# Performance work log

Measured on AMD Instinct MI355X. Metric: run time of the kernel, lower is better.

The kernel has to match this reference:

```python
import jax, jax.numpy as jnp
import numpy as np
import math

B, S, D, H = 4, 2048, 1024, 16
DK = D // H  # 64


def setup_inputs() -> dict:
    key = jax.random.key(0)
    ks = jax.random.split(key, 10)
    scale = 1.0 / math.sqrt(D)
    inp = {
        "context_sequence": jax.random.normal(ks[0], (B, S, D), dtype=jnp.float32),
        "value_sequence": jax.random.normal(ks[1], (B, S, D), dtype=jnp.float32),
        "mask": jax.random.randint(ks[2], (S, S), 0, 2, dtype=jnp.int32),
        # stacked per-head projection params: [H, D, DK] weights, [H, DK] biases
        "Wq": jax.random.uniform(ks[3], (H, D, DK), jnp.float32, -scale, scale),
        "bq": jnp.zeros((H, DK), jnp.float32),
        "Wk": jax.random.uniform(ks[4], (H, D, DK), jnp.float32, -scale, scale),
        "bk": jnp.zeros((H, DK), jnp.float32),
        "Wv": jax.random.uniform(ks[5], (H, D, DK), jnp.float32, -scale, scale),
        "bv": jnp.zeros((H, DK), jnp.float32),
        "Wo": jax.random.uniform(ks[6], (D, D), jnp.float32, -scale, scale),
        "bo": jnp.zeros((D,), jnp.float32),
    }
    return inp


def reference(context_sequence, value_sequence, mask, Wq, bq, Wk, bk, Wv, bv, Wo, bo):
    # per-head projections batched over heads: [B,H,S,DK]
    Q = jnp.einsum("bsd,hdk->bhsk", context_sequence, Wq) + bq[None, :, None, :]
    K = jnp.einsum("bsd,hdk->bhsk", context_sequence, Wk) + bk[None, :, None, :]
    V = jnp.einsum("bsd,hdk->bhsk", value_sequence, Wv) + bv[None, :, None, :]
    scores = jnp.einsum("bhsk,bhtk->bhst", Q, K) / math.sqrt(DK)
    scores = jnp.where(mask[None, None, :, :] == 1, jnp.float32(-1e9), scores)
    attn = jax.nn.softmax(scores, axis=-1)
    out = jnp.einsum("bhst,bhtk->bhsk", attn, V)  # [B,H,S,DK]
    concat = out.transpose(0, 2, 1, 3).reshape(B, S, D)  # heads concatenated
    # output projection (dropout is identity in eval mode)
    return concat @ Wo.T + bo
```

## Files before the change

kernel.cpp:

```cpp
#include <hip/hip_runtime.h>
#include <hip/hip_bf16.h>

#define DEVI __device__ __forceinline__

typedef __attribute__((ext_vector_type(8))) short bf16x8;
typedef __attribute__((ext_vector_type(4))) float f32x4;
typedef unsigned short u16;
typedef unsigned long long u64;


DEVI void async16(const void* g, const void* l) {
  __builtin_amdgcn_global_load_lds(
      (const __attribute__((address_space(1))) unsigned int*)g,
      (__attribute__((address_space(3))) unsigned int*)l, 16, 0, 0);
}

DEVI u16 f2bf(float x) {
  unsigned int u = __float_as_uint(x);
  return (u16)((u + 0x7fffu + ((u >> 16) & 1u)) >> 16);
}

DEVI float fast_exp2(float x) {
#if __has_builtin(__builtin_amdgcn_exp2f)
  return __builtin_amdgcn_exp2f(x);
#else
  return exp2f(x);
#endif
}

DEVI unsigned pk_bf16(unsigned hi, unsigned lo) {
#if __has_builtin(__builtin_amdgcn_perm)
  return __builtin_amdgcn_perm(hi, lo, 0x07060302u);
#else
  return (hi & 0xffff0000u) | (lo >> 16);
#endif
}

DEVI unsigned mk2(unsigned b, int k) {
  return ((((b >> k) & 1u) ? 0u : 0x0000FFFFu) | (((b >> (k + 1)) & 1u) ? 0u : 0xFFFF0000u));
}


__global__ __launch_bounds__(256) void prep_kernel(
    const float* __restrict__ ctx, const float* __restrict__ val, const int* __restrict__ msk,
    const float* __restrict__ Wq, const float* __restrict__ Wk, const float* __restrict__ Wv,
    const float* __restrict__ Wo, const float* __restrict__ bq, const float* __restrict__ bk,
    u16* __restrict__ Xc, u16* __restrict__ Xv, u16* __restrict__ Wqt, u16* __restrict__ Wkt,
    u16* __restrict__ Wvt, u16* __restrict__ WoB, u64* __restrict__ mbits, float* __restrict__ bqk) {
  __shared__ float tile[64 * 69];
  const int blk = blockIdx.x, tid = threadIdx.x;
  if (blk < 16384) {
    const float* src = (blk < 8192) ? ctx : val;
    u16* dst = (blk < 8192) ? Xc : Xv;
    int i = (blk & 8191) * 256 + tid;
    float4 v = ((const float4*)src)[i];
    ushort4 o;
    o.x = f2bf(v.x); o.y = f2bf(v.y); o.z = f2bf(v.z); o.w = f2bf(v.w);
    ((ushort4*)dst)[i] = o;
  } else if (blk < 17408) {
    int i = (blk - 16384) * 256 + tid;
    float4 v = ((const float4*)Wo)[i];
    ushort4 o;
    o.x = f2bf(v.x); o.y = f2bf(v.y); o.z = f2bf(v.z); o.w = f2bf(v.w);
    ((ushort4*)WoB)[i] = o;
  } else if (blk < 18176) {
    int t = blk - 17408;
    int mat = t >> 8, r = t & 255, h = r >> 4, d0 = (r & 15) * 64;
    const float* Ws = (mat == 0) ? Wq : (mat == 1) ? Wk : Wv;
    u16* Wd = (mat == 0) ? Wqt : (mat == 1) ? Wkt : Wvt;
    const int dg = tid & 15, rg = tid >> 4;
#pragma unroll
    for (int i = 0; i < 4; i++) {
      int dr = rg + i * 16;
      float4 v = *(const float4*)&Ws[((size_t)(h * 1024 + d0 + dr)) * 64 + dg * 4];
      tile[dr * 69 + dg * 4 + 0] = v.x;
      tile[dr * 69 + dg * 4 + 1] = v.y;
      tile[dr * 69 + dg * 4 + 2] = v.z;
      tile[dr * 69 + dg * 4 + 3] = v.w;
    }
    __syncthreads();
#pragma unroll
    for (int i = 0; i < 4; i++) {
      int k = rg + i * 16;
      ushort4 o;
      o.x = f2bf(tile[(dg * 4 + 0) * 69 + k]);
      o.y = f2bf(tile[(dg * 4 + 1) * 69 + k]);
      o.z = f2bf(tile[(dg * 4 + 2) * 69 + k]);
      o.w = f2bf(tile[(dg * 4 + 3) * 69 + k]);
      *(ushort4*)&Wd[(size_t)(h * 64 + k) * 1024 + d0 + dg * 4] = o;
    }
  } else if (blk < 34560) {
    int gid = (blk - 18176) * 256 + tid;
    u64 bal = __ballot(msk[gid] == 1);
    if ((tid & 63) == 0) mbits[(size_t)((gid >> 6) & 31) * 2048 + (gid >> 11)] = bal;
  } else {
    int i = (blk - 34560) * 256 + tid;
    bqk[i] = (i < 1024) ? bq[i] : bk[i - 1024];
  }
}


__global__ __launch_bounds__(256) void qkv_gemm(const u16* __restrict__ Xc, const u16* __restrict__ Xv,
                                                const u16* __restrict__ Wqkt, const u16* __restrict__ Wvt,
                                                const float* __restrict__ bqk, const float* __restrict__ bvv,
                                                u16* __restrict__ QKb, u16* __restrict__ Vtg, float qscale) {
  __shared__ __align__(16) u16 As[128 * 32];
  __shared__ __align__(16) u16 Bs[128 * 32];
  const int tid = threadIdx.x;
  const int w = tid >> 6, lane = tid & 63, quad = lane >> 4, lc = lane & 15;
  const int K = 1024;
  const bool isV = blockIdx.y >= 16;
  const int m0 = blockIdx.x * 128;
  const int n0 = (isV ? (blockIdx.y - 16) : blockIdx.y) * 128;
  const u16* A  = isV ? Xv : Xc;
  const u16* Bt = isV ? Wvt : Wqkt;
  const float* bias = isV ? bvv : bqk;
  const int wrow = (w >> 1) * 64, wcol = (w & 1) * 64;
  const int srow = tid >> 2, sc = tid & 3;
  const u16* Ag = A + (size_t)(m0 + srow) * K + sc * 8;
  const u16* Bg = Bt + (size_t)(n0 + srow) * K + sc * 8;
  u16* Asw = As + w * 512;
  u16* Bsw = Bs + w * 512;

  f32x4 acc[4][4] = {};
  for (int k0 = 0; k0 < K; k0 += 32) {
    async16(Ag + k0, Asw);
    async16(Ag + k0 + (size_t)64 * K, Asw + 2048);
    async16(Bg + k0, Bsw);
    async16(Bg + k0 + (size_t)64 * K, Bsw + 2048);
    __syncthreads();
    bf16x8 af[4], bfr[4];
#pragma unroll
    for (int rt = 0; rt < 4; rt++) af[rt] = *(const bf16x8*)&As[(wrow + rt * 16 + lc) * 32 + quad * 8];
#pragma unroll
    for (int ct = 0; ct < 4; ct++) bfr[ct] = *(const bf16x8*)&Bs[(wcol + ct * 16 + lc) * 32 + quad * 8];
#pragma unroll
    for (int rt = 0; rt < 4; rt++)
#pragma unroll
      for (int ct = 0; ct < 4; ct++)
        acc[rt][ct] = __builtin_amdgcn_mfma_f32_16x16x32_bf16(af[rt], bfr[ct], acc[rt][ct], 0, 0, 0);
    __syncthreads();
  }
#pragma unroll
  for (int ct = 0; ct < 4; ct++) {
    int col = n0 + wcol + ct * 16 + lc;
    float bv = bias[col];
    float os = (!isV && col < 1024) ? qscale : 1.0f;
#pragma unroll
    for (int rt = 0; rt < 4; rt++) {
      if (isV) {
        int trow = m0 + wrow + rt * 16 + quad * 4;
        ushort4 pk;
        pk.x = f2bf(acc[rt][ct][0] + bv);
        pk.y = f2bf(acc[rt][ct][1] + bv);
        pk.z = f2bf(acc[rt][ct][2] + bv);
        pk.w = f2bf(acc[rt][ct][3] + bv);
        size_t off = ((size_t)(trow >> 11) * 1024 + col) * 2048 + (trow & 2047);
        *(ushort4*)(Vtg + off) = pk;
      } else {
#pragma unroll
        for (int r = 0; r < 4; r++) {
          int row = m0 + wrow + rt * 16 + quad * 4 + r;
          QKb[(size_t)row * 2048 + col] = f2bf((acc[rt][ct][r] + bv) * os);
        }
      }
    }
  }
}


__global__ __launch_bounds__(256, 4) void attn_kernel(const u16* __restrict__ QK, const u16* __restrict__ Vt,
                                                      const u64* __restrict__ mbits, u16* __restrict__ AO) {
  __shared__ __align__(16) u16 Ks[2][4096];
  __shared__ __align__(16) u16 Vs[2][4096];
  __shared__ uint4 Tbl[256];
  const int S = 2048, D = 1024, QS = 2048;
  const int tid = threadIdx.x, w = tid >> 6, lane = tid & 63, quad = lane >> 4, lc = lane & 15;
  const int q0 = blockIdx.x * 128;
  const int b = blockIdx.y >> 4, h = blockIdx.y & 15;
  const size_t baseq = (size_t)b * S * QS + (size_t)h * 64;
  const size_t vbase = (size_t)blockIdx.y * 64 * S;
  const int sr = lane >> 3, gch = (lane & 7) ^ sr, lx = lc & 7;
  u16* Ksq = (u16*)Ks;

  {
    unsigned bv = (unsigned)tid;
    uint4 e;
    e.x = mk2(bv, 0); e.y = mk2(bv, 2); e.z = mk2(bv, 4); e.w = mk2(bv, 6);
    Tbl[bv] = e;
  }

#pragma unroll
  for (int i = 0; i < 4; i++) {
    const u16* g = QK + baseq + (size_t)(q0 + w * 32 + i * 8 + sr) * QS + gch * 8;
    async16(g, Ksq + w * 2048 + i * 512);
  }
  const int kperm = 32 * (w & 1) + 4 * (w >> 1) + 8 * (sr >> 2) + (sr & 3);
  const u16* Kg0 = QK + baseq + 1024 + (size_t)kperm * QS + gch * 8;
  const u16* Vg0 = Vt + vbase + (size_t)(w * 16 + sr) * S + gch * 8;
  __syncthreads();

  bf16x8 aq[2][2];
#pragma unroll
  for (int s = 0; s < 2; s++)
#pragma unroll
    for (int ks = 0; ks < 2; ks++)
      aq[s][ks] = *(const bf16x8*)&Ksq[w * 2048 + (s * 16 + lc) * 64 + (((ks * 4 + quad) ^ lx) << 3)];
  __syncthreads();

  async16(Kg0, Ks[0] + w * 1024);
  async16(Kg0 + (size_t)16 * QS, Ks[0] + w * 1024 + 512);
  async16(Vg0, Vs[0] + w * 1024);
  async16(Vg0 + (size_t)8 * S, Vs[0] + w * 1024 + 512);

  const u64* mptr = mbits + (size_t)(q0 + w * 32 + lc);
  const int sh8 = quad << 3;

  bf16x8 ones;
#pragma unroll
  for (int j = 0; j < 8; j++) ones[j] = (short)0x3F80;

  const f32x4 z = {};
  f32x4 acco[2][4] = {};
  f32x4 accl[2] = {};

  for (int t0 = 0; t0 < S; t0 += 64) {
    const int cur = (t0 >> 6) & 1;
    __syncthreads();
    if (t0 + 64 < S) {
      const u16* Kg = Kg0 + (size_t)(t0 + 64) * QS;
      const u16* Vg = Vg0 + (t0 + 64);
      async16(Kg, Ks[cur ^ 1] + w * 1024);
      async16(Kg + (size_t)16 * QS, Ks[cur ^ 1] + w * 1024 + 512);
      async16(Vg, Vs[cur ^ 1] + w * 1024);
      async16(Vg + (size_t)8 * S, Vs[cur ^ 1] + w * 1024 + 512);
    }

    u64 mw0 = mptr[(size_t)(t0 >> 6) * 2048];
    u64 mw1 = mptr[(size_t)(t0 >> 6) * 2048 + 16];

    f32x4 sacc[2][4];
    __builtin_amdgcn_s_setprio(1);
#pragma unroll
    for (int ct = 0; ct < 4; ct++) {
      bf16x8 bk = *(const bf16x8*)&Ks[cur][(ct * 16 + lc) * 64 + ((quad ^ lx) << 3)];
      sacc[0][ct] = __builtin_amdgcn_mfma_f32_16x16x32_bf16(bk, aq[0][0], z, 0, 0, 0);
      sacc[1][ct] = __builtin_amdgcn_mfma_f32_16x16x32_bf16(bk, aq[1][0], z, 0, 0, 0);
    }
#pragma unroll
    for (int ct = 0; ct < 4; ct++) {
      bf16x8 bk = *(const bf16x8*)&Ks[cur][(ct * 16 + lc) * 64 + (((4 + quad) ^ lx) << 3)];
      sacc[0][ct] = __builtin_amdgcn_mfma_f32_16x16x32_bf16(bk, aq[0][1], sacc[0][ct], 0, 0, 0);
      sacc[1][ct] = __builtin_amdgcn_mfma_f32_16x16x32_bf16(bk, aq[1][1], sacc[1][ct], 0, 0, 0);
    }
    __builtin_amdgcn_s_setprio(0);

#pragma unroll
    for (int s = 0; s < 2; s++) {
      const u64 mw = s ? mw1 : mw0;
      uint4 ma = Tbl[((unsigned)mw >> sh8) & 255u];
      uint4 mb = Tbl[((unsigned)(mw >> 32) >> sh8) & 255u];
      unsigned pu[4][4];
#pragma unroll
      for (int ct = 0; ct < 4; ct++)
#pragma unroll
        for (int r = 0; r < 4; r++)
          pu[ct][r] = __float_as_uint(fast_exp2(sacc[s][ct][r]));
      union { unsigned u[4]; bf16x8 v; } f0, f1;
      f0.u[0] = pk_bf16(pu[0][1], pu[0][0]) & ma.x;
      f0.u[1] = pk_bf16(pu[0][3], pu[0][2]) & ma.y;
      f0.u[2] = pk_bf16(pu[2][1], pu[2][0]) & ma.z;
      f0.u[3] = pk_bf16(pu[2][3], pu[2][2]) & ma.w;
      f1.u[0] = pk_bf16(pu[1][1], pu[1][0]) & mb.x;
      f1.u[1] = pk_bf16(pu[1][3], pu[1][2]) & mb.y;
      f1.u[2] = pk_bf16(pu[3][1], pu[3][0]) & mb.z;
      f1.u[3] = pk_bf16(pu[3][3], pu[3][2]) & mb.w;

      __builtin_amdgcn_s_setprio(1);
#pragma unroll
      for (int ct = 0; ct < 4; ct++) {
        bf16x8 bv = *(const bf16x8*)&Vs[cur][(ct * 16 + lc) * 64 + ((quad ^ lx) << 3)];
        acco[s][ct] = __builtin_amdgcn_mfma_f32_16x16x32_bf16(f0.v, bv, acco[s][ct], 0, 0, 0);
      }
      accl[s] = __builtin_amdgcn_mfma_f32_16x16x32_bf16(f0.v, ones, accl[s], 0, 0, 0);
#pragma unroll
      for (int ct = 0; ct < 4; ct++) {
        bf16x8 bv = *(const bf16x8*)&Vs[cur][(ct * 16 + lc) * 64 + (((4 + quad) ^ lx) << 3)];
        acco[s][ct] = __builtin_amdgcn_mfma_f32_16x16x32_bf16(f1.v, bv, acco[s][ct], 0, 0, 0);
      }
      accl[s] = __builtin_amdgcn_mfma_f32_16x16x32_bf16(f1.v, ones, accl[s], 0, 0, 0);
      __builtin_amdgcn_s_setprio(0);
    }
  }

#pragma unroll
  for (int s = 0; s < 2; s++)
#pragma unroll
    for (int r = 0; r < 4; r++) {
      float inv = 1.0f / accl[s][r];
      size_t row = (size_t)b * S + q0 + w * 32 + s * 16 + quad * 4 + r;
#pragma unroll
      for (int ct = 0; ct < 4; ct++)
        AO[row * D + h * 64 + ct * 16 + lc] = f2bf(acco[s][ct][r] * inv);
    }
}


__global__ __launch_bounds__(256) void out_gemm(const u16* __restrict__ A, const u16* __restrict__ Bt,
                                                const float* __restrict__ bias, float* __restrict__ C) {
  __shared__ __align__(16) u16 As[128 * 32];
  __shared__ __align__(16) u16 Bs[128 * 32];
  const int tid = threadIdx.x;
  const int w = tid >> 6, lane = tid & 63, quad = lane >> 4, lc = lane & 15;
  const int K = 1024, N = 1024;
  const int m0 = blockIdx.x * 128, n0 = blockIdx.y * 128;
  const int wrow = (w >> 1) * 64, wcol = (w & 1) * 64;
  const int srow = tid >> 2, sc = tid & 3;
  const u16* Ag = A + (size_t)(m0 + srow) * K + sc * 8;
  const u16* Bg = Bt + (size_t)(n0 + srow) * K + sc * 8;
  u16* Asw = As + w * 512;
  u16* Bsw = Bs + w * 512;

  f32x4 acc[4][4] = {};
  for (int k0 = 0; k0 < K; k0 += 32) {
    async16(Ag + k0, Asw);
    async16(Ag + k0 + (size_t)64 * K, Asw + 2048);
    async16(Bg + k0, Bsw);
    async16(Bg + k0 + (size_t)64 * K, Bsw + 2048);
    __syncthreads();
    bf16x8 af[4], bfr[4];
#pragma unroll
    for (int rt = 0; rt < 4; rt++) af[rt] = *(const bf16x8*)&As[(wrow + rt * 16 + lc) * 32 + quad * 8];
#pragma unroll
    for (int ct = 0; ct < 4; ct++) bfr[ct] = *(const bf16x8*)&Bs[(wcol + ct * 16 + lc) * 32 + quad * 8];
#pragma unroll
    for (int rt = 0; rt < 4; rt++)
#pragma unroll
      for (int ct = 0; ct < 4; ct++)
        acc[rt][ct] = __builtin_amdgcn_mfma_f32_16x16x32_bf16(af[rt], bfr[ct], acc[rt][ct], 0, 0, 0);
    __syncthreads();
  }
#pragma unroll
  for (int ct = 0; ct < 4; ct++) {
    int col = n0 + wcol + ct * 16 + lc;
    float bv = bias[col];
#pragma unroll
    for (int rt = 0; rt < 4; rt++)
#pragma unroll
      for (int r = 0; r < 4; r++) {
        int row = m0 + wrow + rt * 16 + quad * 4 + r;
        C[(size_t)row * N + col] = acc[rt][ct][r] + bv;
      }
  }
}


extern "C" void kernel_launch(void* const* d_in, const int* in_sizes, int n_in,
                              void* d_out, int out_size, void* d_ws, size_t ws_size,
                              hipStream_t stream) {
  const int B = 4, S = 2048, D = 1024;
  const float* ctx = (const float*)d_in[0];
  const float* val = (const float*)d_in[1];
  const int*   msk = (const int*)d_in[2];
  const float* Wq  = (const float*)d_in[3];
  const float* bq  = (const float*)d_in[4];
  const float* Wk  = (const float*)d_in[5];
  const float* bk  = (const float*)d_in[6];
  const float* Wv  = (const float*)d_in[7];
  const float* bv  = (const float*)d_in[8];
  const float* Wo  = (const float*)d_in[9];
  const float* bo  = (const float*)d_in[10];
  float* out = (float*)d_out;

  char* ws = (char*)d_ws;
  size_t off = 0;
  auto alloc = [&](size_t sz) { void* p = ws + off; off += (sz + 255) & ~255ULL; return p; };
  const size_t NTOK = (size_t)B * S * D;
  u16* Xc  = (u16*)alloc(NTOK * 2);
  u16* Xv  = (u16*)alloc(NTOK * 2);
  u16* Wqt = (u16*)alloc((size_t)D * D * 2);
  u16* Wkt = (u16*)alloc((size_t)D * D * 2);
  u16* Wvt = (u16*)alloc((size_t)D * D * 2);
  u16* WoB = (u16*)alloc((size_t)D * D * 2);
  u16* QKb = (u16*)alloc(NTOK * 4);
  u16* Vtg = (u16*)alloc(NTOK * 2);
  u64* mbits = (u64*)alloc((size_t)S * S / 8);
  float* bqk = (float*)alloc(2048 * 4);
  u16* AO = Xc;
  if (off > ws_size) return;

  const float qscale = 0.125f * 1.44269504088896f;

  prep_kernel<<<34568, 256, 0, stream>>>(ctx, val, msk, Wq, Wk, Wv, Wo, bq, bk,
                                         Xc, Xv, Wqt, Wkt, Wvt, WoB, mbits, bqk);

  qkv_gemm<<<dim3(B * S / 128, 24), 256, 0, stream>>>(Xc, Xv, Wqt, Wvt, bqk, bv, QKb, Vtg, qscale);

  attn_kernel<<<dim3(S / 128, B * 16), 256, 0, stream>>>(QKb, Vtg, mbits, AO);

  out_gemm<<<dim3(B * S / 128, D / 128), 256, 0, stream>>>(AO, WoB, bo, out);
}
```

Before: 340.9 us.

## Double attention query tile per block to 256 rows and hoist V fragments

Each attention block now handles 256 query rows (64 per wave) instead of 128, so every K/V tile loaded into LDS is reused across twice as many queries, and the grid is halved. V fragments are read from LDS once per tile into registers and reused across all four 16-row sub-tiles. The Q staging buffer and the K/V double buffers now share one LDS array. The cost is higher register pressure (launch bounds drop to 2 blocks) and fewer blocks, which may reduce occupancy and latency hiding.

```diff
diff --git a/kernel.cpp b/kernel.cpp
--- a/kernel.cpp
+++ b/kernel.cpp
@@ -169,19 +169,17 @@
 }
 
 
-__global__ __launch_bounds__(256, 4) void attn_kernel(const u16* __restrict__ QK, const u16* __restrict__ Vt,
+__global__ __launch_bounds__(256, 2) void attn_kernel(const u16* __restrict__ QK, const u16* __restrict__ Vt,
                                                       const u64* __restrict__ mbits, u16* __restrict__ AO) {
-  __shared__ __align__(16) u16 Ks[2][4096];
-  __shared__ __align__(16) u16 Vs[2][4096];
+  __shared__ __align__(16) u16 SM[16384];
   __shared__ uint4 Tbl[256];
   const int S = 2048, D = 1024, QS = 2048;
   const int tid = threadIdx.x, w = tid >> 6, lane = tid & 63, quad = lane >> 4, lc = lane & 15;
-  const int q0 = blockIdx.x * 128;
+  const int q0 = blockIdx.x * 256;
   const int b = blockIdx.y >> 4, h = blockIdx.y & 15;
   const size_t baseq = (size_t)b * S * QS + (size_t)h * 64;
   const size_t vbase = (size_t)blockIdx.y * 64 * S;
   const int sr = lane >> 3, gch = (lane & 7) ^ sr, lx = lc & 7;
-  u16* Ksq = (u16*)Ks;
 
   {
     unsigned bv = (unsigned)tid;
@@ -191,29 +189,29 @@
   }
 
 #pragma unroll
-  for (int i = 0; i < 4; i++) {
-    const u16* g = QK + baseq + (size_t)(q0 + w * 32 + i * 8 + sr) * QS + gch * 8;
-    async16(g, Ksq + w * 2048 + i * 512);
+  for (int i = 0; i < 8; i++) {
+    const u16* g = QK + baseq + (size_t)(q0 + w * 64 + i * 8 + sr) * QS + gch * 8;
+    async16(g, SM + w * 4096 + i * 512);
   }
   const int kperm = 32 * (w & 1) + 4 * (w >> 1) + 8 * (sr >> 2) + (sr & 3);
   const u16* Kg0 = QK + baseq + 1024 + (size_t)kperm * QS + gch * 8;
   const u16* Vg0 = Vt + vbase + (size_t)(w * 16 + sr) * S + gch * 8;
   __syncthreads();
 
-  bf16x8 aq[2][2];
-#pragma unroll
-  for (int s = 0; s < 2; s++)
+  bf16x8 aq[4][2];
+#pragma unroll
+  for (int s = 0; s < 4; s++)
 #pragma unroll
     for (int ks = 0; ks < 2; ks++)
-      aq[s][ks] = *(const bf16x8*)&Ksq[w * 2048 + (s * 16 + lc) * 64 + (((ks * 4 + quad) ^ lx) << 3)];
+      aq[s][ks] = *(const bf16x8*)&SM[w * 4096 + (s * 16 + lc) * 64 + (((ks * 4 + quad) ^ lx) << 3)];
   __syncthreads();
 
-  async16(Kg0, Ks[0] + w * 1024);
-  async16(Kg0 + (size_t)16 * QS, Ks[0] + w * 1024 + 512);
-  async16(Vg0, Vs[0] + w * 1024);
-  async16(Vg0 + (size_t)8 * S, Vs[0] + w * 1024 + 512);
-
-  const u64* mptr = mbits + (size_t)(q0 + w * 32 + lc);
+  async16(Kg0, SM + w * 1024);
+  async16(Kg0 + (size_t)16 * QS, SM + w * 1024 + 512);
+  async16(Vg0, SM + 8192 + w * 1024);
+  async16(Vg0 + (size_t)8 * S, SM + 8192 + w * 1024 + 512);
+
+  const u64* mptr = mbits + (size_t)(q0 + w * 64 + lc);
   const int sh8 = quad << 3;
 
   bf16x8 ones;
@@ -221,84 +219,98 @@
   for (int j = 0; j < 8; j++) ones[j] = (short)0x3F80;
 
   const f32x4 z = {};
-  f32x4 acco[2][4] = {};
-  f32x4 accl[2] = {};
+  f32x4 acco[4][4] = {};
+  f32x4 accl[4] = {};
 
   for (int t0 = 0; t0 < S; t0 += 64) {
     const int cur = (t0 >> 6) & 1;
+    const u16* Kc = SM + cur * 4096;
+    const u16* Vc = SM + 8192 + cur * 4096;
     __syncthreads();
     if (t0 + 64 < S) {
+      u16* Kn = SM + (cur ^ 1) * 4096;
+      u16* Vn = SM + 8192 + (cur ^ 1) * 4096;
       const u16* Kg = Kg0 + (size_t)(t0 + 64) * QS;
       const u16* Vg = Vg0 + (t0 + 64);
-      async16(Kg, Ks[cur ^ 1] + w * 1024);
-      async16(Kg + (size_t)16 * QS, Ks[cur ^ 1] + w * 1024 + 512);
-      async16(Vg, Vs[cur ^ 1] + w * 1024);
-      async16(Vg + (size_t)8 * S, Vs[cur ^ 1] + w * 1024 + 512);
+      async16(Kg, Kn + w * 1024);
+      async16(Kg + (size_t)16 * QS, Kn + w * 1024 + 512);
+      async16(Vg, Vn + w * 1024);
+      async16(Vg + (size_t)8 * S, Vn + w * 1024 + 512);
     }
 
     u64 mw0 = mptr[(size_t)(t0 >> 6) * 2048];
     u64 mw1 = mptr[(size_t)(t0 >> 6) * 2048 + 16];
-
-    f32x4 sacc[2][4];
-    __builtin_amdgcn_s_setprio(1);
+    u64 mw2 = mptr[(size_t)(t0 >> 6) * 2048 + 32];
+    u64 mw3 = mptr[(size_t)(t0 >> 6) * 2048 + 48];
+
+    bf16x8 bv0[4], bv1[4];
 #pragma unroll
     for (int ct = 0; ct < 4; ct++) {
-      bf16x8 bk = *(const bf16x8*)&Ks[cur][(ct * 16 + lc) * 64 + ((quad ^ lx) << 3)];
-      sacc[0][ct] = __builtin_amdgcn_mfma_f32_16x16x32_bf16(bk, aq[0][0], z, 0, 0, 0);
-      sacc[1][ct] = __builtin_amdgcn_mfma_f32_16x16x32_bf16(bk, aq[1][0], z, 0, 0, 0);
-    }
-#pragma unroll
-    for (int ct = 0; ct < 4; ct++) {
-      bf16x8 bk = *(const bf16x8*)&Ks[cur][(ct * 16 + lc) * 64 + (((4 + quad) ^ lx) << 3)];
-      sacc[0][ct] = __builtin_amdgcn_mfma_f32_16x16x32_bf16(bk, aq[0][1], sacc[0][ct], 0, 0, 0);
-      sacc[1][ct] = __builtin_amdgcn_mfma_f32_16x16x32_bf16(bk, aq[1][1], sacc[1][ct], 0, 0, 0);
-    }
-    __builtin_amdgcn_s_setprio(0);
-
-#pragma unroll
-    for (int s = 0; s < 2; s++) {
-      const u64 mw = s ? mw1 : mw0;
-      uint4 ma = Tbl[((unsigned)mw >> sh8) & 255u];
-      uint4 mb = Tbl[((unsigned)(mw >> 32) >> sh8) & 255u];
-      unsigned pu[4][4];
-#pragma unroll
-      for (int ct = 0; ct < 4; ct++)
-#pragma unroll
-        for (int r = 0; r < 4; r++)
-          pu[ct][r] = __float_as_uint(fast_exp2(sacc[s][ct][r]));
-      union { unsigned u[4]; bf16x8 v; } f0, f1;
-      f0.u[0] = pk_bf16(pu[0][1], pu[0][0]) & ma.x;
-      f0.u[1] = pk_bf16(pu[0][3], pu[0][2]) & ma.y;
-      f0.u[2] = pk_bf16(pu[2][1], pu[2][0]) & ma.z;
-      f0.u[3] = pk_bf16(pu[2][3], pu[2][2]) & ma.w;
-      f1.u[0] = pk_bf16(pu[1][1], pu[1][0]) & mb.x;
-      f1.u[1] = pk_bf16(pu[1][3], pu[1][2]) & mb.y;
-      f1.u[2] = pk_bf16(pu[3][1], pu[3][0]) & mb.z;
-      f1.u[3] = pk_bf16(pu[3][3], pu[3][2]) & mb.w;
-
+      bv0[ct] = *(const bf16x8*)&Vc[(ct * 16 + lc) * 64 + ((quad ^ lx) << 3)];
+      bv1[ct] = *(const bf16x8*)&Vc[(ct * 16 + lc) * 64 + (((4 + quad) ^ lx) << 3)];
+    }
+
+#pragma unroll
+    for (int rnd = 0; rnd < 2; rnd++) {
+      const int s0 = rnd * 2;
+      f32x4 sacc[2][4];
       __builtin_amdgcn_s_setprio(1);
 #pragma unroll
       for (int ct = 0; ct < 4; ct++) {
-        bf16x8 bv = *(const bf16x8*)&Vs[cur][(ct * 16 + lc) * 64 + ((quad ^ lx) << 3)];
-        acco[s][ct] = __builtin_amdgcn_mfma_f32_16x16x32_bf16(f0.v, bv, acco[s][ct], 0, 0, 0);
+        bf16x8 bk = *(const bf16x8*)&Kc[(ct * 16 + lc) * 64 + ((quad ^ lx) << 3)];
+        sacc[0][ct] = __builtin_amdgcn_mfma_f32_16x16x32_bf16(bk, aq[s0][0], z, 0, 0, 0);
+        sacc[1][ct] = __builtin_amdgcn_mfma_f32_16x16x32_bf16(bk, aq[s0 + 1][0], z, 0, 0, 0);
       }
-      accl[s] = __builtin_amdgcn_mfma_f32_16x16x32_bf16(f0.v, ones, accl[s], 0, 0, 0);
 #pragma unroll
       for (int ct = 0; ct < 4; ct++) {
-        bf16x8 bv = *(const bf16x8*)&Vs[cur][(ct * 16 + lc) * 64 + (((4 + quad) ^ lx) << 3)];
-        acco[s][ct] = __builtin_amdgcn_mfma_f32_16x16x32_bf16(f1.v, bv, acco[s][ct], 0, 0, 0);
+        bf16x8 bk = *(const bf16x8*)&Kc[(ct * 16 + lc) * 64 + (((4 + quad) ^ lx) << 3)];
+        sacc[0][ct] = __builtin_amdgcn_mfma_f32_16x16x32_bf16(bk, aq[s0][1], sacc[0][ct], 0, 0, 0);
+        sacc[1][ct] = __builtin_amdgcn_mfma_f32_16x16x32_bf16(bk, aq[s0 + 1][1], sacc[1][ct], 0, 0, 0);
       }
-      accl[s] = __builtin_amdgcn_mfma_f32_16x16x32_bf16(f1.v, ones, accl[s], 0, 0, 0);
       __builtin_amdgcn_s_setprio(0);
-    }
-  }
-
-#pragma unroll
-  for (int s = 0; s < 2; s++)
+
+#pragma unroll
+      for (int si = 0; si < 2; si++) {
+        const int s = s0 + si;
+        const u64 mw = (s == 0) ? mw0 : (s == 1) ? mw1 : (s == 2) ? mw2 : mw3;
+        uint4 ma = Tbl[((unsigned)mw >> sh8) & 255u];
+        uint4 mb = Tbl[((unsigned)(mw >> 32) >> sh8) & 255u];
+        unsigned pu[4][4];
+#pragma unroll
+        for (int ct = 0; ct < 4; ct++)
+#pragma unroll
+          for (int r = 0; r < 4; r++)
+            pu[ct][r] = __float_as_uint(fast_exp2(sacc[si][ct][r]));
+        union { unsigned u[4]; bf16x8 v; } f0, f1;
+        f0.u[0] = pk_bf16(pu[0][1], pu[0][0]) & ma.x;
+        f0.u[1] = pk_bf16(pu[0][3], pu[0][2]) & ma.y;
+        f0.u[2] = pk_bf16(pu[2][1], pu[2][0]) & ma.z;
+        f0.u[3] = pk_bf16(pu[2][3], pu[2][2]) & ma.w;
+        f1.u[0] = pk_bf16(pu[1][1], pu[1][0]) & mb.x;
+        f1.u[1] = pk_bf16(pu[1][3], pu[1][2]) & mb.y;
+        f1.u[2] = pk_bf16(pu[3][1], pu[3][0]) & mb.z;
+        f1.u[3] = pk_bf16(pu[3][3], pu[3][2]) & mb.w;
+
+        __builtin_amdgcn_s_setprio(1);
+#pragma unroll
+        for (int ct = 0; ct < 4; ct++)
+          acco[s][ct] = __builtin_amdgcn_mfma_f32_16x16x32_bf16(f0.v, bv0[ct], acco[s][ct], 0, 0, 0);
+        accl[s] = __builtin_amdgcn_mfma_f32_16x16x32_bf16(f0.v, ones, accl[s], 0, 0, 0);
+#pragma unroll
+        for (int ct = 0; ct < 4; ct++)
+          acco[s][ct] = __builtin_amdgcn_mfma_f32_16x16x32_bf16(f1.v, bv1[ct], acco[s][ct], 0, 0, 0);
+        accl[s] = __builtin_amdgcn_mfma_f32_16x16x32_bf16(f1.v, ones, accl[s], 0, 0, 0);
+        __builtin_amdgcn_s_setprio(0);
+      }
+    }
+  }
+
+#pragma unroll
+  for (int s = 0; s < 4; s++)
 #pragma unroll
     for (int r = 0; r < 4; r++) {
       float inv = 1.0f / accl[s][r];
-      size_t row = (size_t)b * S + q0 + w * 32 + s * 16 + quad * 4 + r;
+      size_t row = (size_t)b * S + q0 + w * 64 + s * 16 + quad * 4 + r;
 #pragma unroll
       for (int ct = 0; ct < 4; ct++)
         AO[row * D + h * 64 + ct * 16 + lc] = f2bf(acco[s][ct][r] * inv);
@@ -396,7 +408,7 @@
 
   qkv_gemm<<<dim3(B * S / 128, 24), 256, 0, stream>>>(Xc, Xv, Wqt, Wvt, bqk, bv, QKb, Vtg, qscale);
 
-  attn_kernel<<<dim3(S / 128, B * 16), 256, 0, stream>>>(QKb, Vtg, mbits, AO);
+  attn_kernel<<<dim3(S / 256, B * 16), 256, 0, stream>>>(QKb, Vtg, mbits, AO);
 
   out_gemm<<<dim3(B * S / 128, D / 128), 256, 0, stream>>>(AO, WoB, bo, out);
 }
```

Result: faster. 332.9 us (-2.3%).
